# Optimization experiments

Measured on AMD Instinct MI355X. Metric: run time of the kernel, lower is better.

## Reference

```python
import jax, jax.numpy as jnp
import numpy as np

N = 50000
E = 800000
HID = 32
HEADS = 8
OUT_DIM = 16
NEG_SLOPE = 0.2
LN_EPS = 1e-5


def setup_inputs() -> dict:
    key = jax.random.key(0)
    ks = jax.random.split(key, 32)
    rn = lambda k, shape, s=0.1: (jax.random.normal(k, shape, jnp.float32) * s)
    d = {}
    d['x'] = jax.random.normal(ks[0], (N, 1), jnp.float32)
    d['edge_index'] = jax.random.randint(ks[1], (2, E), 0, N, dtype=jnp.int64)
    d['batch'] = jnp.zeros((N,), dtype=jnp.int64)
    # in_layer: Linear(1, HID)
    d['Win'] = rn(ks[2], (1, HID)); d['bin_'] = rn(ks[3], (HID,))
    # layer 0: residual Linear(HID, HID*HEADS), GATConv(HID -> HID, heads=HEADS, concat)
    d['Wr0'] = rn(ks[4], (HID, HID * HEADS)); d['br0'] = rn(ks[5], (HID * HEADS,))
    d['W0'] = rn(ks[6], (HID, HID * HEADS))
    d['as0'] = rn(ks[7], (HEADS, HID)); d['ad0'] = rn(ks[8], (HEADS, HID))
    d['bg0'] = rn(ks[9], (HID * HEADS,))
    d['g0'] = jnp.ones((HID * HEADS,), jnp.float32); d['b0'] = jnp.zeros((HID * HEADS,), jnp.float32)
    # layer 1: residual Linear(HID*HEADS, HID), GATConv(HID*HEADS -> HID, heads=1, concat=False)
    d['Wr1'] = rn(ks[10], (HID * HEADS, HID)); d['br1'] = rn(ks[11], (HID,))
    d['W1'] = rn(ks[12], (HID * HEADS, HID))
    d['as1'] = rn(ks[13], (1, HID)); d['ad1'] = rn(ks[14], (1, HID))
    d['bg1'] = rn(ks[15], (HID,))
    d['g1'] = jnp.ones((HID,), jnp.float32); d['b1'] = jnp.zeros((HID,), jnp.float32)
    # out_layer: Linear(HID, OUT_DIM)
    d['Wout'] = rn(ks[16], (HID, OUT_DIM)); d['bout'] = rn(ks[17], (OUT_DIM,))
    return d


def _layer_norm(x, g, b):
    m = x.mean(-1, keepdims=True)
    v = ((x - m) ** 2).mean(-1, keepdims=True)
    return (x - m) * jax.lax.rsqrt(v + LN_EPS) * g + b


def _gat_conv(x, src, dst, W, att_src, att_dst, bias, heads, n):
    # x: [n, in]; W: [in, heads*out]; att_*: [heads, out]
    h = (x @ W).reshape(n, heads, -1)                      # [n, H, F]
    a_s = (h * att_src).sum(-1)                            # [n, H]
    a_d = (h * att_dst).sum(-1)                            # [n, H]
    e = jax.nn.leaky_relu(a_s[src] + a_d[dst], NEG_SLOPE)  # [E', H]
    emax = jax.ops.segment_max(e, dst, num_segments=n)
    ex = jnp.exp(e - emax[dst])
    denom = jax.ops.segment_sum(ex, dst, num_segments=n)
    alpha = ex / (denom[dst] + 1e-16)                      # segment softmax per dst node
    out = jax.ops.segment_sum(h[src] * alpha[..., None], dst, num_segments=n)  # [n, H, F]
    return out.reshape(n, -1) + bias                       # concat heads (heads=1 -> mean=identity)


def reference(x, edge_index, batch, Win, bin_, Wr0, br0, W0, as0, ad0, bg0, g0, b0,
              Wr1, br1, W1, as1, ad1, bg1, g1, b1, Wout, bout):
    n = x.shape[0]
    loop = jnp.arange(n, dtype=edge_index.dtype)
    src = jnp.concatenate([edge_index[0], loop])  # PyG GATConv add_self_loops=True
    dst = jnp.concatenate([edge_index[1], loop])

    h = x @ Win + bin_                                       # [n, HID]
    # layer 0
    res = h @ Wr0 + br0
    h = _gat_conv(h, src, dst, W0, as0, ad0, bg0, HEADS, n)  # [n, HID*HEADS]
    h = jax.nn.elu(h)                                        # not last layer
    h = _layer_norm(h + res, g0, b0)
    # layer 1 (last)
    res = h @ Wr1 + br1
    h = _gat_conv(h, src, dst, W1, as1, ad1, bg1, 1, n)      # [n, HID]
    h = _layer_norm(h + res, g1, b1)
    # global mean pool
    n_graphs = 1
    sums = jax.ops.segment_sum(h, batch, num_segments=n_graphs)
    cnts = jax.ops.segment_sum(jnp.ones((n, 1), h.dtype), batch, num_segments=n_graphs)
    pooled = sums / cnts                                     # [1, HID]
    return pooled @ Wout + bout                              # [1, OUT_DIM]
```

## Files before the change

kernel.cpp:

```cpp
#include <hip/hip_runtime.h>
#include <hip/hip_fp16.h>
#include <math.h>

#define N_NODES 50000
#define N_EDGES 800000
#define HEADS 8
#define OUTD 16
#define NEG_SLOPE 0.2f
#define LN_EPS 1e-5f
#define NB0 196
#define NEGBIG -3.0e38f
#define PADDEG 64
#define NPOOL 64
#define SC_CHUNK 2048
#define SC_NCHUNK ((N_EDGES + SC_CHUNK - 1) / SC_CHUNK)
#define NGRAN 3125
#define NBLK_REMAP 12512

typedef _Float16 half8 __attribute__((ext_vector_type(8)));
typedef float f32x4 __attribute__((ext_vector_type(4)));

__device__ __forceinline__ int remap_base(int b, bool& ok) {
    int p = b & 7, q = b >> 3;
    int c = (q >> 2) * 8 + p;
    ok = (c < NGRAN);
    return c * 16 + (q & 3) * 4;
}

__global__ __launch_bounds__(256) void k_prep(const float* __restrict__ Win,
    const float* __restrict__ bin, const float* __restrict__ Wr0,
    const float* __restrict__ br0, const float* __restrict__ W0,
    const float* __restrict__ as0, const float* __restrict__ ad0,
    const float* __restrict__ Wr1, const float* __restrict__ W1,
    float* __restrict__ tab, float* __restrict__ tabPQRS,
    _Float16* __restrict__ wpk,
    int* __restrict__ cnt, float* __restrict__ partial) {
    const int t = threadIdx.x;
    const int bx = blockIdx.x;
    const int tid = bx * 256 + t;
    if (tid < N_NODES) cnt[tid] = 0;
    if (tid < NPOOL * 32) partial[tid] = 0.f;
    if (bx >= 1 && bx <= 64) {
        int idx = (bx - 1) * 256 + t;
        int j = idx & 7;
        int n = (idx >> 3) & 63;
        int qk = idx >> 9;
        int k = qk * 8 + j;
        float wv = (n < 32) ? Wr1[k * 32 + n] : W1[k * 32 + (n - 32)];
        wpk[idx] = (_Float16)wv;
    }
    if (bx != 0) return;
    __shared__ float sA1[256], sB1[256];
    float a0 = 0.f, b0 = 0.f, a1 = 0.f, b1 = 0.f;
#pragma unroll
    for (int k = 0; k < 32; k++) {
        float wk = Win[k], bk = bin[k];
        float wr = Wr0[k * 256 + t];
        float ww = W0[k * 256 + t];
        a0 = fmaf(wk, wr, a0); b0 = fmaf(bk, wr, b0);
        a1 = fmaf(wk, ww, a1); b1 = fmaf(bk, ww, b1);
    }
    b0 += br0[t];
    sA1[t] = a1; sB1[t] = b1;
    tab[t] = a0; tab[256 + t] = b0; tab[512 + t] = a1; tab[768 + t] = b1;
    __syncthreads();
    if (t < 8) {
        float P = 0.f, Q = 0.f, R = 0.f, S = 0.f;
        for (int c = 0; c < 32; c++) {
            float aw = sA1[t * 32 + c], bw = sB1[t * 32 + c];
            float av = as0[t * 32 + c], dv = ad0[t * 32 + c];
            P = fmaf(aw, av, P); Q = fmaf(bw, av, Q);
            R = fmaf(aw, dv, R); S = fmaf(bw, dv, S);
        }
        tabPQRS[t] = P; tabPQRS[8 + t] = Q; tabPQRS[16 + t] = R; tabPQRS[24 + t] = S;
    }
}

__global__ __launch_bounds__(256) void k_scatter(const int* __restrict__ srcA,
    const int* __restrict__ dstA, int* cnt, unsigned short* __restrict__ csrp) {
    const int phase = blockIdx.x & 7;
    const int chunk = blockIdx.x >> 3;
    const int4* __restrict__ d4p = (const int4*)dstA;
    const int f0 = chunk * (SC_CHUNK / 4) + threadIdx.x;
#pragma unroll
    for (int k = 0; k < 2; k++) {
        int f = f0 + k * 256;
        int e0 = f * 4;
        if (e0 < N_EDGES) {
            int4 dv = d4p[f];
            int dd[4] = {dv.x, dv.y, dv.z, dv.w};
#pragma unroll
            for (int u = 0; u < 4; u++) {
                int d = dd[u];
                if (((d >> 4) & 7) == phase) {
                    int p = atomicAdd(&cnt[d], 1);
                    if (p < PADDEG - 1) csrp[d * PADDEG + p] = (unsigned short)srcA[e0 + u];
                }
            }
        }
    }
}

__global__ __launch_bounds__(256) void k_agg0(const int* __restrict__ cnt,
    const unsigned short* __restrict__ csrp, const float* __restrict__ x,
    const float* __restrict__ tab, const float* __restrict__ tabPQRS,
    const float* __restrict__ bg0, const float* __restrict__ g0,
    const float* __restrict__ b0, __half* __restrict__ h1out) {
    bool ok;
    const int base = remap_base(blockIdx.x, ok);
    if (!ok) return;
    const int t = threadIdx.x;
    const int w = t >> 6, l = t & 63;
    const int i = base + w;
    const int slot = l >> 3, h = l & 7;
    const int row = i * PADDEG;
    const int total = min(cnt[i], PADDEG - 1) + 1;
    const float xi = x[i];
    const float P = tabPQRS[h];
    const float C = tabPQRS[8 + h] + fmaf(xi, tabPQRS[16 + h], tabPQRS[24 + h]);
    float psum = 0.f, pxsum = 0.f;
#pragma unroll
    for (int k = 0; k < 8; k++) {
        int idx = slot + k * 8;
        if (idx >= total) break;
        int s = (idx == 0) ? i : (int)csrp[row + idx - 1];
        float xs = x[s];
        float e = fmaf(P, xs, C);
        e = (e > 0.f) ? e : NEG_SLOPE * e;
        float p = __expf(e);
        psum += p;
        pxsum = fmaf(p, xs, pxsum);
    }
    psum += __shfl_xor(psum, 8);   pxsum += __shfl_xor(pxsum, 8);
    psum += __shfl_xor(psum, 16);  pxsum += __shfl_xor(pxsum, 16);
    psum += __shfl_xor(psum, 32);  pxsum += __shfl_xor(pxsum, 32);
    const int hl = l >> 3;
    const float Ph  = __shfl(psum, hl);
    const float PXh = __shfl(pxsum, hl);
    const float inv = 1.f / (Ph + 1e-16f);
    const float Xh = PXh * inv;
    const float Sh = Ph * inv;
    const int c = l * 4;
    float4 A0v = *(const float4*)(tab + c);
    float4 B0v = *(const float4*)(tab + 256 + c);
    float4 A1v = *(const float4*)(tab + 512 + c);
    float4 B1v = *(const float4*)(tab + 768 + c);
    float4 bg = *(const float4*)(bg0 + c);
    float val[4];
    val[0] = fmaf(A1v.x, Xh, fmaf(B1v.x, Sh, bg.x));
    val[1] = fmaf(A1v.y, Xh, fmaf(B1v.y, Sh, bg.y));
    val[2] = fmaf(A1v.z, Xh, fmaf(B1v.z, Sh, bg.z));
    val[3] = fmaf(A1v.w, Xh, fmaf(B1v.w, Sh, bg.w));
#pragma unroll
    for (int k = 0; k < 4; k++) val[k] = (val[k] > 0.f) ? val[k] : (__expf(val[k]) - 1.f);
    val[0] += fmaf(xi, A0v.x, B0v.x);
    val[1] += fmaf(xi, A0v.y, B0v.y);
    val[2] += fmaf(xi, A0v.z, B0v.z);
    val[3] += fmaf(xi, A0v.w, B0v.w);
    float sm = val[0] + val[1] + val[2] + val[3];
#pragma unroll
    for (int o = 1; o <= 32; o <<= 1) sm += __shfl_xor(sm, o);
    float mean = sm * (1.f / 256.f);
    float d[4], vv = 0.f;
#pragma unroll
    for (int k = 0; k < 4; k++) { d[k] = val[k] - mean; vv = fmaf(d[k], d[k], vv); }
#pragma unroll
    for (int o = 1; o <= 32; o <<= 1) vv += __shfl_xor(vv, o);
    float rstd = rsqrtf(vv * (1.f / 256.f) + LN_EPS);
    float4 gv = *(const float4*)(g0 + c);
    float4 bv = *(const float4*)(b0 + c);
    __half2 o0 = __float22half2_rn(make_float2(fmaf(d[0] * rstd, gv.x, bv.x),
                                               fmaf(d[1] * rstd, gv.y, bv.y)));
    __half2 o1 = __float22half2_rn(make_float2(fmaf(d[2] * rstd, gv.z, bv.z),
                                               fmaf(d[3] * rstd, gv.w, bv.w)));
    uint2 ou;
    ou.x = *(unsigned*)&o0; ou.y = *(unsigned*)&o1;
    *(uint2*)(h1out + (size_t)i * 256 + c) = ou;
}

__global__ __launch_bounds__(256) void k_lin1(const __half* __restrict__ h1h,
    const _Float16* __restrict__ wpk, const float* __restrict__ br1,
    const float* __restrict__ as1, const float* __restrict__ ad1,
    __half* __restrict__ res1h, __half* __restrict__ hW1h,
    float* __restrict__ a_s1, float* __restrict__ a_d1) {
    const int t = threadIdx.x;
    const int w = t >> 6, l = t & 63;
    const int q = l >> 4;
    const int col = l & 15;
    const int nodeA = blockIdx.x * 64 + w * 16 + col;
    const half8* __restrict__ Bg = (const half8*)wpk;
    f32x4 c0 = {0.f, 0.f, 0.f, 0.f}, c1 = c0, c2 = c0, c3 = c0;
#pragma unroll
    for (int kt = 0; kt < 8; kt++) {
        half8 a = {0,0,0,0,0,0,0,0};
        if (nodeA < N_NODES)
            a = *(const half8*)(h1h + (size_t)nodeA * 256 + kt * 32 + q * 8);
        const int bb = (kt * 4 + q) * 64 + col;
        half8 b0 = Bg[bb +  0];
        half8 b1 = Bg[bb + 16];
        half8 b2 = Bg[bb + 32];
        half8 b3 = Bg[bb + 48];
        c0 = __builtin_amdgcn_mfma_f32_16x16x32_f16(a, b0, c0, 0, 0, 0);
        c1 = __builtin_amdgcn_mfma_f32_16x16x32_f16(a, b1, c1, 0, 0, 0);
        c2 = __builtin_amdgcn_mfma_f32_16x16x32_f16(a, b2, c2, 0, 0, 0);
        c3 = __builtin_amdgcn_mfma_f32_16x16x32_f16(a, b3, c3, 0, 0, 0);
    }
    const int nodeE = blockIdx.x * 64 + w * 16 + q * 4;
    const float brv0 = br1[col], brv1 = br1[col + 16];
    const float asv0 = as1[col], asv1 = as1[col + 16];
    const float adv0 = ad1[col], adv1 = ad1[col + 16];
    float ps[4], pd[4];
#pragma unroll
    for (int r = 0; r < 4; r++) {
        int nd = nodeE + r;
        if (nd < N_NODES) {
            res1h[nd * 32 + col]      = __float2half(c0[r] + brv0);
            res1h[nd * 32 + col + 16] = __float2half(c1[r] + brv1);
            hW1h[nd * 32 + col]      = __float2half(c2[r]);
            hW1h[nd * 32 + col + 16] = __float2half(c3[r]);
        }
        ps[r] = c2[r] * asv0 + c3[r] * asv1;
        pd[r] = c2[r] * adv0 + c3[r] * adv1;
    }
#pragma unroll
    for (int o = 1; o <= 8; o <<= 1) {
#pragma unroll
        for (int r = 0; r < 4; r++) {
            ps[r] += __shfl_xor(ps[r], o);
            pd[r] += __shfl_xor(pd[r], o);
        }
    }
    if (col == 0) {
#pragma unroll
        for (int r = 0; r < 4; r++) {
            int nd = nodeE + r;
            if (nd < N_NODES) { a_s1[nd] = ps[r]; a_d1[nd] = pd[r]; }
        }
    }
}

__global__ __launch_bounds__(256) void k_agg1(const int* __restrict__ cnt,
    const unsigned short* __restrict__ csrp, const float* __restrict__ a_s1,
    const float* __restrict__ a_d1, const __half* __restrict__ hW1h,
    const float* __restrict__ bg1, const __half* __restrict__ res1h,
    const float* __restrict__ g1, const float* __restrict__ b1,
    float* __restrict__ partial) {
    bool ok;
    const int base = remap_base(blockIdx.x, ok);
    if (!ok) return;
    const int t = threadIdx.x;
    const int w = t >> 6, l = t & 63;
    const int i = base + w;
    const int row = i * PADDEG;
    const int total = min(cnt[i], PADDEG - 1) + 1;
    const float ad = a_d1[i];
    const bool valid = (l < total);
    int sl = i;
    if (valid && l > 0) sl = (int)csrp[row + l - 1];
    float pl = 0.f;
    if (valid) {
        float e = a_s1[sl] + ad;
        e = (e > 0.f) ? e : NEG_SLOPE * e;
        pl = __expf(e);
    }
    float lsum = pl;
#pragma unroll
    for (int o = 1; o <= 32; o <<= 1) lsum += __shfl_xor(lsum, o);
    const float inv = 1.f / (lsum + 1e-16f);
    const int slot = l >> 3, u = l & 7;
    float4 acc = make_float4(0.f, 0.f, 0.f, 0.f);
    for (int idx = slot; idx < total; idx += 8) {
        int s = __shfl(sl, idx);
        float p = __shfl(pl, idx);
        uint2 uu = *(const uint2*)(hW1h + (size_t)s * 32 + u * 4);
        float2 v0 = __half22float2(*(const __half2*)&uu.x);
        float2 v1 = __half22float2(*(const __half2*)&uu.y);
        acc.x = fmaf(p, v0.x, acc.x); acc.y = fmaf(p, v0.y, acc.y);
        acc.z = fmaf(p, v1.x, acc.z); acc.w = fmaf(p, v1.y, acc.w);
    }
#pragma unroll
    for (int o = 8; o <= 32; o <<= 1) {
        acc.x += __shfl_xor(acc.x, o); acc.y += __shfl_xor(acc.y, o);
        acc.z += __shfl_xor(acc.z, o); acc.w += __shfl_xor(acc.w, o);
    }
    float4 bg = *(const float4*)(bg1 + u * 4);
    uint2 ru = *(const uint2*)(res1h + (size_t)i * 32 + u * 4);
    float2 rr0 = __half22float2(*(const __half2*)&ru.x);
    float2 rr1 = __half22float2(*(const __half2*)&ru.y);
    float4 val;
    val.x = fmaf(acc.x, inv, bg.x) + rr0.x; val.y = fmaf(acc.y, inv, bg.y) + rr0.y;
    val.z = fmaf(acc.z, inv, bg.z) + rr1.x; val.w = fmaf(acc.w, inv, bg.w) + rr1.y;
    float sm = val.x + val.y + val.z + val.w;
    sm += __shfl_xor(sm, 1); sm += __shfl_xor(sm, 2); sm += __shfl_xor(sm, 4);
    float mean = sm * (1.f / 32.f);
    float4 d;
    d.x = val.x - mean; d.y = val.y - mean; d.z = val.z - mean; d.w = val.w - mean;
    float vv = d.x * d.x + d.y * d.y + d.z * d.z + d.w * d.w;
    vv += __shfl_xor(vv, 1); vv += __shfl_xor(vv, 2); vv += __shfl_xor(vv, 4);
    float rstd = rsqrtf(vv * (1.f / 32.f) + LN_EPS);
    float4 gv = *(const float4*)(g1 + u * 4);
    float4 bv = *(const float4*)(b1 + u * 4);
    float4 outv;
    outv.x = fmaf(d.x * rstd, gv.x, bv.x); outv.y = fmaf(d.y * rstd, gv.y, bv.y);
    outv.z = fmaf(d.z * rstd, gv.z, bv.z); outv.w = fmaf(d.w * rstd, gv.w, bv.w);
    __shared__ float sp[4][32];
    if (l < 8) *(float4*)(&sp[w][u * 4]) = outv;
    __syncthreads();
    if (t < 32) {
        float s = sp[0][t] + sp[1][t] + sp[2][t] + sp[3][t];
        atomicAdd(&partial[(blockIdx.x & (NPOOL - 1)) * 32 + t], s);
    }
}

__global__ __launch_bounds__(64) void k_final(const float* __restrict__ partial,
                                              const float* __restrict__ Wout,
                                              const float* __restrict__ bout,
                                              float* __restrict__ out) {
    __shared__ float pooled[32];
    int t = threadIdx.x;
    if (t < 32) {
        float a = 0.f;
        for (int b = 0; b < NPOOL; b++) a += partial[b * 32 + t];
        pooled[t] = a * (1.f / (float)N_NODES);
    }
    __syncthreads();
    if (t < OUTD) {
        float o = bout[t];
        for (int c = 0; c < 32; c++) o = fmaf(pooled[c], Wout[c * OUTD + t], o);
        out[t] = o;
    }
}

extern "C" void kernel_launch(void* const* d_in, const int* in_sizes, int n_in,
                              void* d_out, int out_size, void* d_ws, size_t ws_size,
                              hipStream_t stream) {
    const float* x    = (const float*)d_in[0];
    const int*   eidx = (const int*)d_in[1];
    const float* Win  = (const float*)d_in[3];
    const float* bin  = (const float*)d_in[4];
    const float* Wr0  = (const float*)d_in[5];
    const float* br0  = (const float*)d_in[6];
    const float* W0   = (const float*)d_in[7];
    const float* as0  = (const float*)d_in[8];
    const float* ad0  = (const float*)d_in[9];
    const float* bg0  = (const float*)d_in[10];
    const float* g0   = (const float*)d_in[11];
    const float* b0   = (const float*)d_in[12];
    const float* Wr1  = (const float*)d_in[13];
    const float* br1  = (const float*)d_in[14];
    const float* W1   = (const float*)d_in[15];
    const float* as1  = (const float*)d_in[16];
    const float* ad1  = (const float*)d_in[17];
    const float* bg1  = (const float*)d_in[18];
    const float* g1   = (const float*)d_in[19];
    const float* b1   = (const float*)d_in[20];
    const float* Wout = (const float*)d_in[21];
    const float* bout = (const float*)d_in[22];
    float* out = (float*)d_out;

    const int* srcA = eidx;
    const int* dstA = eidx + N_EDGES;

    char* B = (char*)d_ws;
    __half* h1h = (__half*)B;
    __half* res1h = (__half*)(B + 25600000);
    _Float16* wpk = (_Float16*)(B + 28900000);
    __half* hW1h = (__half*)(B + 29600000);
    float* a_s1  = (float*)(B + 33600000);
    float* a_d1  = (float*)(B + 33900000);
    unsigned short* csrp = (unsigned short*)(B + 34200000);
    int* cnt     = (int*)(B + 40600000);
    float* partial = (float*)(B + 40900000);
    float* tab   = (float*)(B + 40910000);
    float* tabPQRS = (float*)(B + 40915000);

    k_prep<<<NB0, 256, 0, stream>>>(Win, bin, Wr0, br0, W0, as0, ad0, Wr1, W1,
                                    tab, tabPQRS, wpk, cnt, partial);
    k_scatter<<<SC_NCHUNK * 8, 256, 0, stream>>>(srcA, dstA, cnt, csrp);
    k_agg0<<<NBLK_REMAP, 256, 0, stream>>>(cnt, csrp, x, tab, tabPQRS,
                                           bg0, g0, b0, h1h);
    k_lin1<<<(N_NODES + 63) / 64, 256, 0, stream>>>(h1h, wpk, br1, as1, ad1,
                                                    res1h, hW1h, a_s1, a_d1);
    k_agg1<<<NBLK_REMAP, 256, 0, stream>>>(cnt, csrp, a_s1, a_d1, hW1h,
                                           bg1, res1h, g1, b1, partial);
    k_final<<<1, 64, 0, stream>>>(partial, Wout, bout, out);
}
```

Baseline: 205.5 us.

## Fuse layer-0 aggregation with layer-1 linear via shared-memory fp16 tile

Merges the layer-0 attention aggregation/LayerNorm kernel and the layer-1 MFMA linear kernel into one 1024-thread block. Each block computes 16 nodes' 256-wide normalized features, stores them in a swizzled LDS tile, and one wavefront runs the MFMA projection from LDS. This removes the 25.6 MB fp16 intermediate write and re-read plus a kernel launch. In exchange, 15 of 16 waves sit idle during the MFMA phase, the XCD-aware block remap is dropped, and the larger blocks may lower occupancy.

Measured after the change: 201.1 us. 2.1% less time.

```diff
diff --git a/kernel.cpp b/kernel.cpp
--- a/kernel.cpp
+++ b/kernel.cpp
@@ -101,111 +101,110 @@
     }
 }
 
-__global__ __launch_bounds__(256) void k_agg0(const int* __restrict__ cnt,
+__global__ __launch_bounds__(1024) void k_agg0f(const int* __restrict__ cnt,
     const unsigned short* __restrict__ csrp, const float* __restrict__ x,
     const float* __restrict__ tab, const float* __restrict__ tabPQRS,
     const float* __restrict__ bg0, const float* __restrict__ g0,
-    const float* __restrict__ b0, __half* __restrict__ h1out) {
-    bool ok;
-    const int base = remap_base(blockIdx.x, ok);
-    if (!ok) return;
-    const int t = threadIdx.x;
-    const int w = t >> 6, l = t & 63;
-    const int i = base + w;
-    const int slot = l >> 3, h = l & 7;
-    const int row = i * PADDEG;
-    const int total = min(cnt[i], PADDEG - 1) + 1;
-    const float xi = x[i];
-    const float P = tabPQRS[h];
-    const float C = tabPQRS[8 + h] + fmaf(xi, tabPQRS[16 + h], tabPQRS[24 + h]);
-    float psum = 0.f, pxsum = 0.f;
-#pragma unroll
-    for (int k = 0; k < 8; k++) {
-        int idx = slot + k * 8;
-        if (idx >= total) break;
-        int s = (idx == 0) ? i : (int)csrp[row + idx - 1];
-        float xs = x[s];
-        float e = fmaf(P, xs, C);
-        e = (e > 0.f) ? e : NEG_SLOPE * e;
-        float p = __expf(e);
-        psum += p;
-        pxsum = fmaf(p, xs, pxsum);
-    }
-    psum += __shfl_xor(psum, 8);   pxsum += __shfl_xor(pxsum, 8);
-    psum += __shfl_xor(psum, 16);  pxsum += __shfl_xor(pxsum, 16);
-    psum += __shfl_xor(psum, 32);  pxsum += __shfl_xor(pxsum, 32);
-    const int hl = l >> 3;
-    const float Ph  = __shfl(psum, hl);
-    const float PXh = __shfl(pxsum, hl);
-    const float inv = 1.f / (Ph + 1e-16f);
-    const float Xh = PXh * inv;
-    const float Sh = Ph * inv;
-    const int c = l * 4;
-    float4 A0v = *(const float4*)(tab + c);
-    float4 B0v = *(const float4*)(tab + 256 + c);
-    float4 A1v = *(const float4*)(tab + 512 + c);
-    float4 B1v = *(const float4*)(tab + 768 + c);
-    float4 bg = *(const float4*)(bg0 + c);
-    float val[4];
-    val[0] = fmaf(A1v.x, Xh, fmaf(B1v.x, Sh, bg.x));
-    val[1] = fmaf(A1v.y, Xh, fmaf(B1v.y, Sh, bg.y));
-    val[2] = fmaf(A1v.z, Xh, fmaf(B1v.z, Sh, bg.z));
-    val[3] = fmaf(A1v.w, Xh, fmaf(B1v.w, Sh, bg.w));
-#pragma unroll
-    for (int k = 0; k < 4; k++) val[k] = (val[k] > 0.f) ? val[k] : (__expf(val[k]) - 1.f);
-    val[0] += fmaf(xi, A0v.x, B0v.x);
-    val[1] += fmaf(xi, A0v.y, B0v.y);
-    val[2] += fmaf(xi, A0v.z, B0v.z);
-    val[3] += fmaf(xi, A0v.w, B0v.w);
-    float sm = val[0] + val[1] + val[2] + val[3];
-#pragma unroll
-    for (int o = 1; o <= 32; o <<= 1) sm += __shfl_xor(sm, o);
-    float mean = sm * (1.f / 256.f);
-    float d[4], vv = 0.f;
-#pragma unroll
-    for (int k = 0; k < 4; k++) { d[k] = val[k] - mean; vv = fmaf(d[k], d[k], vv); }
-#pragma unroll
-    for (int o = 1; o <= 32; o <<= 1) vv += __shfl_xor(vv, o);
-    float rstd = rsqrtf(vv * (1.f / 256.f) + LN_EPS);
-    float4 gv = *(const float4*)(g0 + c);
-    float4 bv = *(const float4*)(b0 + c);
-    __half2 o0 = __float22half2_rn(make_float2(fmaf(d[0] * rstd, gv.x, bv.x),
-                                               fmaf(d[1] * rstd, gv.y, bv.y)));
-    __half2 o1 = __float22half2_rn(make_float2(fmaf(d[2] * rstd, gv.z, bv.z),
-                                               fmaf(d[3] * rstd, gv.w, bv.w)));
-    uint2 ou;
-    ou.x = *(unsigned*)&o0; ou.y = *(unsigned*)&o1;
-    *(uint2*)(h1out + (size_t)i * 256 + c) = ou;
-}
-
-__global__ __launch_bounds__(256) void k_lin1(const __half* __restrict__ h1h,
+    const float* __restrict__ b0,
     const _Float16* __restrict__ wpk, const float* __restrict__ br1,
     const float* __restrict__ as1, const float* __restrict__ ad1,
     __half* __restrict__ res1h, __half* __restrict__ hW1h,
     float* __restrict__ a_s1, float* __restrict__ a_d1) {
+    const int bid = blockIdx.x;
+    if (bid >= NGRAN) return;
+    const int base = bid * 16;
     const int t = threadIdx.x;
-    const int w = t >> 6, l = t & 63;
+    const int wv = t >> 6, l = t & 63;
+    __shared__ _Float16 hL[16 * 256];
+    {
+        const int i = base + wv;
+        const int slot = l >> 3, h = l & 7;
+        const int row = i * PADDEG;
+        const int total = min(cnt[i], PADDEG - 1) + 1;
+        const float xi = x[i];
+        const float P = tabPQRS[h];
+        const float C = tabPQRS[8 + h] + fmaf(xi, tabPQRS[16 + h], tabPQRS[24 + h]);
+        float psum = 0.f, pxsum = 0.f;
+#pragma unroll
+        for (int k = 0; k < 8; k++) {
+            int idx = slot + k * 8;
+            if (idx >= total) break;
+            int s = (idx == 0) ? i : (int)csrp[row + idx - 1];
+            float xs = x[s];
+            float e = fmaf(P, xs, C);
+            e = (e > 0.f) ? e : NEG_SLOPE * e;
+            float p = __expf(e);
+            psum += p;
+            pxsum = fmaf(p, xs, pxsum);
+        }
+        psum += __shfl_xor(psum, 8);   pxsum += __shfl_xor(pxsum, 8);
+        psum += __shfl_xor(psum, 16);  pxsum += __shfl_xor(pxsum, 16);
+        psum += __shfl_xor(psum, 32);  pxsum += __shfl_xor(pxsum, 32);
+        const int hl = l >> 3;
+        const float Ph  = __shfl(psum, hl);
+        const float PXh = __shfl(pxsum, hl);
+        const float inv = 1.f / (Ph + 1e-16f);
+        const float Xh = PXh * inv;
+        const float Sh = Ph * inv;
+        const int c = l * 4;
+        float4 A0v = *(const float4*)(tab + c);
+        float4 B0v = *(const float4*)(tab + 256 + c);
+        float4 A1v = *(const float4*)(tab + 512 + c);
+        float4 B1v = *(const float4*)(tab + 768 + c);
+        float4 bg = *(const float4*)(bg0 + c);
+        float val[4];
+        val[0] = fmaf(A1v.x, Xh, fmaf(B1v.x, Sh, bg.x));
+        val[1] = fmaf(A1v.y, Xh, fmaf(B1v.y, Sh, bg.y));
+        val[2] = fmaf(A1v.z, Xh, fmaf(B1v.z, Sh, bg.z));
+        val[3] = fmaf(A1v.w, Xh, fmaf(B1v.w, Sh, bg.w));
+#pragma unroll
+        for (int k = 0; k < 4; k++) val[k] = (val[k] > 0.f) ? val[k] : (__expf(val[k]) - 1.f);
+        val[0] += fmaf(xi, A0v.x, B0v.x);
+        val[1] += fmaf(xi, A0v.y, B0v.y);
+        val[2] += fmaf(xi, A0v.z, B0v.z);
+        val[3] += fmaf(xi, A0v.w, B0v.w);
+        float sm = val[0] + val[1] + val[2] + val[3];
+#pragma unroll
+        for (int o = 1; o <= 32; o <<= 1) sm += __shfl_xor(sm, o);
+        float mean = sm * (1.f / 256.f);
+        float d[4], vvv = 0.f;
+#pragma unroll
+        for (int k = 0; k < 4; k++) { d[k] = val[k] - mean; vvv = fmaf(d[k], d[k], vvv); }
+#pragma unroll
+        for (int o = 1; o <= 32; o <<= 1) vvv += __shfl_xor(vvv, o);
+        float rstd = rsqrtf(vvv * (1.f / 256.f) + LN_EPS);
+        float4 gv = *(const float4*)(g0 + c);
+        float4 bv = *(const float4*)(b0 + c);
+        __half2 o0 = __float22half2_rn(make_float2(fmaf(d[0] * rstd, gv.x, bv.x),
+                                                   fmaf(d[1] * rstd, gv.y, bv.y)));
+        __half2 o1 = __float22half2_rn(make_float2(fmaf(d[2] * rstd, gv.z, bv.z),
+                                                   fmaf(d[3] * rstd, gv.w, bv.w)));
+        uint2 ou;
+        ou.x = *(unsigned*)&o0; ou.y = *(unsigned*)&o1;
+        const int ks = (l >> 1) ^ (wv & 7);
+        *(uint2*)(&hL[wv * 256 + ks * 8 + (l & 1) * 4]) = ou;
+    }
+    __syncthreads();
+    if (t >= 64) return;
     const int q = l >> 4;
     const int col = l & 15;
-    const int nodeA = blockIdx.x * 64 + w * 16 + col;
     const half8* __restrict__ Bg = (const half8*)wpk;
     f32x4 c0 = {0.f, 0.f, 0.f, 0.f}, c1 = c0, c2 = c0, c3 = c0;
 #pragma unroll
     for (int kt = 0; kt < 8; kt++) {
-        half8 a = {0,0,0,0,0,0,0,0};
-        if (nodeA < N_NODES)
-            a = *(const half8*)(h1h + (size_t)nodeA * 256 + kt * 32 + q * 8);
+        const int ksr = (kt * 4 + q) ^ (col & 7);
+        half8 a = *(const half8*)(&hL[col * 256 + ksr * 8]);
         const int bb = (kt * 4 + q) * 64 + col;
-        half8 b0 = Bg[bb +  0];
-        half8 b1 = Bg[bb + 16];
-        half8 b2 = Bg[bb + 32];
-        half8 b3 = Bg[bb + 48];
-        c0 = __builtin_amdgcn_mfma_f32_16x16x32_f16(a, b0, c0, 0, 0, 0);
-        c1 = __builtin_amdgcn_mfma_f32_16x16x32_f16(a, b1, c1, 0, 0, 0);
-        c2 = __builtin_amdgcn_mfma_f32_16x16x32_f16(a, b2, c2, 0, 0, 0);
-        c3 = __builtin_amdgcn_mfma_f32_16x16x32_f16(a, b3, c3, 0, 0, 0);
-    }
-    const int nodeE = blockIdx.x * 64 + w * 16 + q * 4;
+        half8 b0v = Bg[bb +  0];
+        half8 b1v = Bg[bb + 16];
+        half8 b2v = Bg[bb + 32];
+        half8 b3v = Bg[bb + 48];
+        c0 = __builtin_amdgcn_mfma_f32_16x16x32_f16(a, b0v, c0, 0, 0, 0);
+        c1 = __builtin_amdgcn_mfma_f32_16x16x32_f16(a, b1v, c1, 0, 0, 0);
+        c2 = __builtin_amdgcn_mfma_f32_16x16x32_f16(a, b2v, c2, 0, 0, 0);
+        c3 = __builtin_amdgcn_mfma_f32_16x16x32_f16(a, b3v, c3, 0, 0, 0);
+    }
+    const int nodeE = base + q * 4;
     const float brv0 = br1[col], brv1 = br1[col + 16];
     const float asv0 = as1[col], asv1 = as1[col + 16];
     const float adv0 = ad1[col], adv1 = ad1[col + 16];
@@ -213,12 +212,10 @@
 #pragma unroll
     for (int r = 0; r < 4; r++) {
         int nd = nodeE + r;
-        if (nd < N_NODES) {
-            res1h[nd * 32 + col]      = __float2half(c0[r] + brv0);
-            res1h[nd * 32 + col + 16] = __float2half(c1[r] + brv1);
-            hW1h[nd * 32 + col]      = __float2half(c2[r]);
-            hW1h[nd * 32 + col + 16] = __float2half(c3[r]);
-        }
+        res1h[nd * 32 + col]      = __float2half(c0[r] + brv0);
+        res1h[nd * 32 + col + 16] = __float2half(c1[r] + brv1);
+        hW1h[nd * 32 + col]      = __float2half(c2[r]);
+        hW1h[nd * 32 + col + 16] = __float2half(c3[r]);
         ps[r] = c2[r] * asv0 + c3[r] * asv1;
         pd[r] = c2[r] * adv0 + c3[r] * adv1;
     }
@@ -234,7 +231,7 @@
 #pragma unroll
         for (int r = 0; r < 4; r++) {
             int nd = nodeE + r;
-            if (nd < N_NODES) { a_s1[nd] = ps[r]; a_d1[nd] = pd[r]; }
+            a_s1[nd] = ps[r]; a_d1[nd] = pd[r];
         }
     }
 }
@@ -362,7 +359,6 @@
     const int* dstA = eidx + N_EDGES;
 
     char* B = (char*)d_ws;
-    __half* h1h = (__half*)B;
     __half* res1h = (__half*)(B + 25600000);
     _Float16* wpk = (_Float16*)(B + 28900000);
     __half* hW1h = (__half*)(B + 29600000);
@@ -377,10 +373,9 @@
     k_prep<<<NB0, 256, 0, stream>>>(Win, bin, Wr0, br0, W0, as0, ad0, Wr1, W1,
                                     tab, tabPQRS, wpk, cnt, partial);
     k_scatter<<<SC_NCHUNK * 8, 256, 0, stream>>>(srcA, dstA, cnt, csrp);
-    k_agg0<<<NBLK_REMAP, 256, 0, stream>>>(cnt, csrp, x, tab, tabPQRS,
-                                           bg0, g0, b0, h1h);
-    k_lin1<<<(N_NODES + 63) / 64, 256, 0, stream>>>(h1h, wpk, br1, as1, ad1,
-                                                    res1h, hW1h, a_s1, a_d1);
+    k_agg0f<<<NGRAN, 1024, 0, stream>>>(cnt, csrp, x, tab, tabPQRS, bg0, g0, b0,
+                                        wpk, br1, as1, ad1,
+                                        res1h, hW1h, a_s1, a_d1);
     k_agg1<<<NBLK_REMAP, 256, 0, stream>>>(cnt, csrp, a_s1, a_d1, hW1h,
                                            bg1, res1h, g1, b1, partial);
     k_final<<<1, 64, 0, stream>>>(partial, Wout, bout, out);
```
